# Kernel optimization log

Hardware: AMD Instinct MI355X
Metric: run time of the kernel (lower is better)

The kernel has to match this reference:

```python
import jax, jax.numpy as jnp
import numpy as np

B, T, I, H = 512, 512, 32, 64


def setup_inputs() -> dict:
    key = jax.random.key(0)
    ks = jax.random.split(key, 11)
    s_i = 1.0 / np.sqrt(H)  # PyTorch GRU init scale
    inp = {
        "x": jax.random.normal(ks[0], (B, T, I), dtype=jnp.float32),
        # layer 0 (input size I), layer 1 (input size H); gate order r,z,n
        "W_ih0": jax.random.uniform(ks[1], (3 * H, I), jnp.float32, -s_i, s_i),
        "W_hh0": jax.random.uniform(ks[2], (3 * H, H), jnp.float32, -s_i, s_i),
        "b_ih0": jax.random.uniform(ks[3], (3 * H,), jnp.float32, -s_i, s_i),
        "b_hh0": jax.random.uniform(ks[4], (3 * H,), jnp.float32, -s_i, s_i),
        "W_ih1": jax.random.uniform(ks[5], (3 * H, H), jnp.float32, -s_i, s_i),
        "W_hh1": jax.random.uniform(ks[6], (3 * H, H), jnp.float32, -s_i, s_i),
        "b_ih1": jax.random.uniform(ks[7], (3 * H,), jnp.float32, -s_i, s_i),
        "b_hh1": jax.random.uniform(ks[8], (3 * H,), jnp.float32, -s_i, s_i),
        "fc_w": jax.random.uniform(ks[9], (1, H), jnp.float32, -s_i, s_i),
        "fc_b": jax.random.uniform(ks[10], (1,), jnp.float32, -s_i, s_i),
    }
    return inp


def gru_layer(x, W_ih, W_hh, b_ih, b_hh):
    """One GRU layer over [B,T,D] -> [B,T,H]. PyTorch gate order r,z,n."""
    h = x.shape[-1] * 0  # placeholder, real H from W_hh
    H_ = W_hh.shape[1]
    # precompute input projections for all timesteps: [B,T,3H]
    gi = jnp.einsum("btd,gd->btg", x, W_ih) + b_ih
    gi = jnp.swapaxes(gi, 0, 1)  # [T,B,3H] for scan

    def step(h_prev, gi_t):
        gh = h_prev @ W_hh.T + b_hh  # [B,3H]
        i_r, i_z, i_n = jnp.split(gi_t, 3, axis=-1)
        h_r, h_z, h_n = jnp.split(gh, 3, axis=-1)
        r = jax.nn.sigmoid(i_r + h_r)
        z = jax.nn.sigmoid(i_z + h_z)
        n = jnp.tanh(i_n + r * h_n)
        h_new = (1.0 - z) * n + z * h_prev
        return h_new, h_new

    h0 = jnp.zeros((x.shape[0], H_), dtype=x.dtype)
    _, ys = jax.lax.scan(step, h0, gi)
    return jnp.swapaxes(ys, 0, 1)  # [B,T,H]


def reference(x, W_ih0, W_hh0, b_ih0, b_hh0, W_ih1, W_hh1, b_ih1, b_hh1, fc_w, fc_b):
    # dropout between layers is inactive in eval mode -> identity
    h1 = gru_layer(x, W_ih0, W_hh0, b_ih0, b_hh0)
    h2 = gru_layer(h1, W_ih1, W_hh1, b_ih1, b_hh1)
    last = h2[:, -1, :]  # [B,H]
    return last @ fc_w.T + fc_b  # [B,1]
```

## Files before the change

### kernel.cpp

```cpp
#include <hip/hip_runtime.h>

typedef _Float16 h2 __attribute__((ext_vector_type(2)));
typedef _Float16 h4 __attribute__((ext_vector_type(4)));
typedef _Float16 h8 __attribute__((ext_vector_type(8)));
typedef float    f4 __attribute__((ext_vector_type(4)));

#define TT 512
#define NB 512
#define II 32
#define HH 64
#define BT 16
#define LROW 72

static __device__ __forceinline__ float fexp2f(float x){ return __builtin_amdgcn_exp2f(x); }
static __device__ __forceinline__ float frcpf(float x){ return __builtin_amdgcn_rcpf(x); }
static __device__ __forceinline__ float sigf(float x){ return frcpf(1.0f + fexp2f(-1.442695040888963f*x)); }
static __device__ __forceinline__ float tanhf_fast(float x){ return 1.0f - 2.0f*frcpf(1.0f + fexp2f(2.885390081777926f*x)); }

struct H8S { h2 a,b,c,d; };
struct H4S { h2 a,b; };
static __device__ __forceinline__ h2 pkrtz(float a, float b){
  return __builtin_bit_cast(h2, __builtin_amdgcn_cvt_pkrtz(a, b));
}
static __device__ __forceinline__ h8 pack8(h2 a, h2 b, h2 c, h2 d){
  H8S s{a,b,c,d}; return __builtin_bit_cast(h8, s);
}
static __device__ __forceinline__ h8 cvt8(float4 a, float4 b){
  return pack8(pkrtz(a.x,a.y), pkrtz(a.z,a.w), pkrtz(b.x,b.y), pkrtz(b.z,b.w));
}
static __device__ __forceinline__ h8 ld8cvt(const float* p){
  return cvt8(((const float4*)p)[0], ((const float4*)p)[1]);
}
static __device__ __forceinline__ f4 mfma16(h8 a, h8 b, f4 c){
  return __builtin_amdgcn_mfma_f32_16x16x32_f16(a, b, c, 0, 0, 0);
}

static __device__ __forceinline__ void phase_barrier(){
  asm volatile("s_waitcnt lgkmcnt(0)" ::: "memory");
  __builtin_amdgcn_s_barrier();
  asm volatile("" ::: "memory");
}

#define GPHASE(DOL0, DOL1, XA, XB, P)                                        \
{                                                                            \
  const _Float16* h0r = &h0L[buf][c*LROW];                                   \
  h8 ba = *(const h8*)(h0r + 8*g);                                           \
  h8 bb = *(const h8*)(h0r + 32 + 8*g);                                      \
  f4 Dr, Dz, Dni, Dnh;                                                       \
  if (DOL1) {                                                                \
    const _Float16* h1r = &h1L[buf][c*LROW];                                 \
    h8 v0 = *(const h8*)(h1r + 8*g);                                         \
    h8 v1 = *(const h8*)(h1r + 32 + 8*g);                                    \
    Dr = brv1; Dz = bzv1; Dni = biv1; Dnh = bhv1;                            \
    Dr  = mfma16(P0[0][0], ba, Dr);   Dr  = mfma16(P0[0][1], bb, Dr);        \
    Dr  = mfma16(P1[0][0], v0, Dr);   Dr  = mfma16(P1[0][1], v1, Dr);        \
    Dz  = mfma16(P0[1][0], ba, Dz);   Dz  = mfma16(P0[1][1], bb, Dz);        \
    Dz  = mfma16(P1[1][0], v0, Dz);   Dz  = mfma16(P1[1][1], v1, Dz);        \
    Dni = mfma16(P0[2][0], ba, Dni);  Dni = mfma16(P0[2][1], bb, Dni);       \
    Dnh = mfma16(P1[2][0], v0, Dnh);  Dnh = mfma16(P1[2][1], v1, Dnh);       \
  }                                                                          \
  if (DOL0) {                                                                \
    h8 bx = cvt8(XA, XB);                                                    \
    f4 Cr = brv0, Cz = bzv0, Cni = biv0, Cnh = bhv0;                         \
    Cr  = mfma16(Ah[0][0], ba, Cr);   Cr  = mfma16(Ah[0][1], bb, Cr);        \
    Cz  = mfma16(Ah[1][0], ba, Cz);   Cz  = mfma16(Ah[1][1], bb, Cz);        \
    Cnh = mfma16(Ah[2][0], ba, Cnh);  Cnh = mfma16(Ah[2][1], bb, Cnh);       \
    Cr  = mfma16(Ax[0], bx, Cr);                                             \
    Cz  = mfma16(Ax[1], bx, Cz);                                             \
    Cni = mfma16(Ax[2], bx, Cni);                                            \
    { const float* pn = xrow + (size_t)(((P)+2 < TT) ? ((P)+2) : (TT-1))*II; \
      XA = ((const float4*)pn)[0];  XB = ((const float4*)pn)[1]; }           \
    _Pragma("unroll")                                                        \
    for (int i = 0; i < 4; ++i){                                             \
      const float r  = sigf(Cr[i]);                                          \
      const float z  = sigf(Cz[i]);                                          \
      const float nn = tanhf_fast(Cni[i] + r*Cnh[i]);                        \
      hp0[i] = nn + z*(hp0[i] - nn);                                         \
    }                                                                        \
    H4S s0{ pkrtz(hp0[0], hp0[1]), pkrtz(hp0[2], hp0[3]) };                  \
    *(h4*)(&h0L[buf^1][c*LROW + j0]) = __builtin_bit_cast(h4, s0);           \
  }                                                                          \
  if (DOL1) {                                                                \
    _Pragma("unroll")                                                        \
    for (int i = 0; i < 4; ++i){                                             \
      const float r  = sigf(Dr[i]);                                          \
      const float z  = sigf(Dz[i]);                                          \
      const float nn = tanhf_fast(Dni[i] + r*Dnh[i]);                        \
      hp1[i] = nn + z*(hp1[i] - nn);                                         \
    }                                                                        \
    H4S s1{ pkrtz(hp1[0], hp1[1]), pkrtz(hp1[2], hp1[3]) };                  \
    *(h4*)(&h1L[buf^1][c*LROW + j0]) = __builtin_bit_cast(h4, s1);           \
  }                                                                          \
  phase_barrier();                                                           \
  buf ^= 1;                                                                  \
}

__global__ __launch_bounds__(256, 1)
void gru2_merged(
    const float* __restrict__ x,
    const float* __restrict__ Wih0, const float* __restrict__ Whh0,
    const float* __restrict__ bih0, const float* __restrict__ bhh0,
    const float* __restrict__ Wih1, const float* __restrict__ Whh1,
    const float* __restrict__ b_ih1, const float* __restrict__ b_hh1,
    const float* __restrict__ fcw, const float* __restrict__ fcb,
    float* __restrict__ out)
{
  const int tid  = threadIdx.x;
  const int w    = tid >> 6;
  const int lane = tid & 63;
  const int c    = lane & 15;
  const int g    = lane >> 4;
  const int b0   = blockIdx.x * BT;

  __shared__ _Float16 h0L[2][16*LROW];
  __shared__ _Float16 h1L[2][16*LROW];
  __shared__ float    fcred[256];

  for (int i = tid; i < 16*LROW; i += 256){
    h0L[0][i] = (_Float16)0; h0L[1][i] = (_Float16)0;
    h1L[0][i] = (_Float16)0; h1L[1][i] = (_Float16)0;
  }

  const int r0 = 16*w + c, r1 = 64 + 16*w + c, r2 = 128 + 16*w + c;
  const int j0 = 16*w + 4*g;

  h8 Ax[3];
  h8 Ah[3][2];
  h8 P0[3][2];
  h8 P1[3][2];
  Ax[0] = ld8cvt(Wih0 + r0*II + 8*g);
  Ax[1] = ld8cvt(Wih0 + r1*II + 8*g);
  Ax[2] = ld8cvt(Wih0 + r2*II + 8*g);
#pragma unroll
  for (int q = 0; q < 2; ++q){
    Ah[0][q] = ld8cvt(Whh0 + r0*HH + 32*q + 8*g);
    Ah[1][q] = ld8cvt(Whh0 + r1*HH + 32*q + 8*g);
    Ah[2][q] = ld8cvt(Whh0 + r2*HH + 32*q + 8*g);
    P0[0][q] = ld8cvt(Wih1 + r0*HH + 32*q + 8*g);
    P0[1][q] = ld8cvt(Wih1 + r1*HH + 32*q + 8*g);
    P0[2][q] = ld8cvt(Wih1 + r2*HH + 32*q + 8*g);
    P1[0][q] = ld8cvt(Whh1 + r0*HH + 32*q + 8*g);
    P1[1][q] = ld8cvt(Whh1 + r1*HH + 32*q + 8*g);
    P1[2][q] = ld8cvt(Whh1 + r2*HH + 32*q + 8*g);
  }

  f4 brv0, bzv0, biv0, bhv0, brv1, bzv1, biv1, bhv1;
#pragma unroll
  for (int i = 0; i < 4; ++i){
    brv0[i] = bih0[j0+i]      + bhh0[j0+i];
    bzv0[i] = bih0[64+j0+i]   + bhh0[64+j0+i];
    biv0[i] = bih0[128+j0+i];
    bhv0[i] = bhh0[128+j0+i];
    brv1[i] = b_ih1[j0+i]     + b_hh1[j0+i];
    bzv1[i] = b_ih1[64+j0+i]  + b_hh1[64+j0+i];
    biv1[i] = b_ih1[128+j0+i];
    bhv1[i] = b_hh1[128+j0+i];
  }

  float hp0[4] = {0.f,0.f,0.f,0.f};
  float hp1[4] = {0.f,0.f,0.f,0.f};

  const float* xrow = x + (size_t)(b0+c)*TT*II + 8*g;
  float4 x0a, x0b, x1a, x1b;
  x0a = ((const float4*)xrow)[0];       x0b = ((const float4*)xrow)[1];
  x1a = ((const float4*)(xrow+II))[0];  x1b = ((const float4*)(xrow+II))[1];

  int buf = 0;
  __syncthreads();

  GPHASE(true, false, x0a, x0b, 0);
  for (int p = 1; p < TT-1; p += 2){
    GPHASE(true, true, x1a, x1b, p);
    GPHASE(true, true, x0a, x0b, p+1);
  }
  GPHASE(true, true, x1a, x1b, TT-1);
  GPHASE(false, true, x0a, x0b, 0);

  {
    float s = fcw[j0]*hp1[0] + fcw[j0+1]*hp1[1] + fcw[j0+2]*hp1[2] + fcw[j0+3]*hp1[3];
    fcred[(w*4 + g)*16 + c] = s;
  }
  __syncthreads();
  if (tid < 16){
    float s = fcb[0];
#pragma unroll
    for (int q = 0; q < 16; ++q) s += fcred[q*16 + tid];
    out[b0 + tid] = s;
  }
}

extern "C" void kernel_launch(void* const* d_in, const int* in_sizes, int n_in,
                              void* d_out, int out_size, void* d_ws, size_t ws_size,
                              hipStream_t stream) {
  const float* x    = (const float*)d_in[0];
  const float* Wih0 = (const float*)d_in[1];
  const float* Whh0 = (const float*)d_in[2];
  const float* bih0 = (const float*)d_in[3];
  const float* bhh0 = (const float*)d_in[4];
  const float* Wih1 = (const float*)d_in[5];
  const float* Whh1 = (const float*)d_in[6];
  const float* bih1 = (const float*)d_in[7];
  const float* bhh1 = (const float*)d_in[8];
  const float* fcw  = (const float*)d_in[9];
  const float* fcb  = (const float*)d_in[10];
  float* out = (float*)d_out;

  gru2_merged<<<dim3(NB/BT), dim3(256), 0, stream>>>(
      x, Wih0, Whh0, bih0, bhh0, Wih1, Whh1, bih1, bhh1, fcw, fcb, out);
}
```

Before: 313.1 us.

## Pack two batch groups per block and replace barriers with LDS flag sync

Each 512-thread block now runs two independent 4-wave groups, each handling 16 batch rows with its own LDS state buffers. The grid shrinks to half as many blocks, so two recurrence chains share one CU. The per-step s_barrier is replaced by a per-group spin on LDS flags, using monotonic phase counters and s_sleep, so one group never waits on the other. The aim is to hide each chain's serial latency by interleaving two chains on the same SIMDs. The cost is CU sharing and polling overhead, and the sleep may add wake-up latency to every step.

```diff
diff --git a/kernel.cpp b/kernel.cpp
--- a/kernel.cpp
+++ b/kernel.cpp
@@ -11,6 +11,7 @@
 #define HH 64
 #define BT 16
 #define LROW 72
+#define HSZ  (16*LROW)
 
 static __device__ __forceinline__ float fexp2f(float x){ return __builtin_amdgcn_exp2f(x); }
 static __device__ __forceinline__ float frcpf(float x){ return __builtin_amdgcn_rcpf(x); }
@@ -35,20 +36,23 @@
   return __builtin_amdgcn_mfma_f32_16x16x32_f16(a, b, c, 0, 0, 0);
 }
 
-static __device__ __forceinline__ void phase_barrier(){
+static __device__ __forceinline__ void group_sync(volatile int* fl, int wt, int lane, int target){
   asm volatile("s_waitcnt lgkmcnt(0)" ::: "memory");
-  __builtin_amdgcn_s_barrier();
+  if (lane == 0) fl[wt] = target;
+  while (!(fl[0] >= target && fl[1] >= target && fl[2] >= target && fl[3] >= target)) {
+    __builtin_amdgcn_s_sleep(1);
+  }
   asm volatile("" ::: "memory");
 }
 
 #define GPHASE(DOL0, DOL1, XA, XB, P)                                        \
 {                                                                            \
-  const _Float16* h0r = &h0L[buf][c*LROW];                                   \
+  const _Float16* h0r = h0B + (size_t)buf*HSZ + c*LROW;                      \
   h8 ba = *(const h8*)(h0r + 8*g);                                           \
   h8 bb = *(const h8*)(h0r + 32 + 8*g);                                      \
   f4 Dr, Dz, Dni, Dnh;                                                       \
   if (DOL1) {                                                                \
-    const _Float16* h1r = &h1L[buf][c*LROW];                                 \
+    const _Float16* h1r = h1B + (size_t)buf*HSZ + c*LROW;                    \
     h8 v0 = *(const h8*)(h1r + 8*g);                                         \
     h8 v1 = *(const h8*)(h1r + 32 + 8*g);                                    \
     Dr = brv1; Dz = bzv1; Dni = biv1; Dnh = bhv1;                            \
@@ -78,7 +82,7 @@
       hp0[i] = nn + z*(hp0[i] - nn);                                         \
     }                                                                        \
     H4S s0{ pkrtz(hp0[0], hp0[1]), pkrtz(hp0[2], hp0[3]) };                  \
-    *(h4*)(&h0L[buf^1][c*LROW + j0]) = __builtin_bit_cast(h4, s0);           \
+    *(h4*)(h0B + (size_t)(buf^1)*HSZ + c*LROW + j0) = __builtin_bit_cast(h4, s0); \
   }                                                                          \
   if (DOL1) {                                                                \
     _Pragma("unroll")                                                        \
@@ -89,14 +93,15 @@
       hp1[i] = nn + z*(hp1[i] - nn);                                         \
     }                                                                        \
     H4S s1{ pkrtz(hp1[0], hp1[1]), pkrtz(hp1[2], hp1[3]) };                  \
-    *(h4*)(&h1L[buf^1][c*LROW + j0]) = __builtin_bit_cast(h4, s1);           \
+    *(h4*)(h1B + (size_t)(buf^1)*HSZ + c*LROW + j0) = __builtin_bit_cast(h4, s1); \
   }                                                                          \
-  phase_barrier();                                                           \
+  ++ph;                                                                      \
+  group_sync(flg, wt, lane, ph);                                             \
   buf ^= 1;                                                                  \
 }
 
-__global__ __launch_bounds__(256, 1)
-void gru2_merged(
+__global__ __launch_bounds__(512, 2)
+void gru2_dual(
     const float* __restrict__ x,
     const float* __restrict__ Wih0, const float* __restrict__ Whh0,
     const float* __restrict__ bih0, const float* __restrict__ bhh0,
@@ -107,22 +112,31 @@
 {
   const int tid  = threadIdx.x;
   const int w    = tid >> 6;
+  const int grp  = w >> 2;
+  const int wt   = w & 3;
   const int lane = tid & 63;
   const int c    = lane & 15;
   const int g    = lane >> 4;
-  const int b0   = blockIdx.x * BT;
-
-  __shared__ _Float16 h0L[2][16*LROW];
-  __shared__ _Float16 h1L[2][16*LROW];
-  __shared__ float    fcred[256];
-
-  for (int i = tid; i < 16*LROW; i += 256){
-    h0L[0][i] = (_Float16)0; h0L[1][i] = (_Float16)0;
-    h1L[0][i] = (_Float16)0; h1L[1][i] = (_Float16)0;
-  }
-
-  const int r0 = 16*w + c, r1 = 64 + 16*w + c, r2 = 128 + 16*w + c;
-  const int j0 = 16*w + 4*g;
+  const int b0   = blockIdx.x * (2*BT) + grp*BT;
+
+  __shared__ _Float16 h0G[2][2][HSZ];
+  __shared__ _Float16 h1G[2][2][HSZ];
+  __shared__ float    fcred[2][256];
+  __shared__ int      flags[2][4];
+
+  for (int i = tid; i < 2*2*HSZ; i += 512){
+    ((_Float16*)h0G)[i] = (_Float16)0;
+    ((_Float16*)h1G)[i] = (_Float16)0;
+  }
+  if (tid < 8) ((int*)flags)[tid] = 0;
+
+  _Float16* h0B = &h0G[grp][0][0];
+  _Float16* h1B = &h1G[grp][0][0];
+  volatile int* flg = &flags[grp][0];
+  int ph = 0;
+
+  const int r0 = 16*wt + c, r1 = 64 + 16*wt + c, r2 = 128 + 16*wt + c;
+  const int j0 = 16*wt + 4*g;
 
   h8 Ax[3];
   h8 Ah[3][2];
@@ -178,14 +192,15 @@
 
   {
     float s = fcw[j0]*hp1[0] + fcw[j0+1]*hp1[1] + fcw[j0+2]*hp1[2] + fcw[j0+3]*hp1[3];
-    fcred[(w*4 + g)*16 + c] = s;
-  }
-  __syncthreads();
-  if (tid < 16){
+    fcred[grp][(wt*4 + g)*16 + c] = s;
+  }
+  ++ph;
+  group_sync(flg, wt, lane, ph);
+  if (wt == 0 && lane < 16){
     float s = fcb[0];
 #pragma unroll
-    for (int q = 0; q < 16; ++q) s += fcred[q*16 + tid];
-    out[b0 + tid] = s;
+    for (int q = 0; q < 16; ++q) s += fcred[grp][q*16 + lane];
+    out[b0 + lane] = s;
   }
 }
 
@@ -205,6 +220,6 @@
   const float* fcb  = (const float*)d_in[10];
   float* out = (float*)d_out;
 
-  gru2_merged<<<dim3(NB/BT), dim3(256), 0, stream>>>(
+  gru2_dual<<<dim3(NB/(2*BT)), dim3(512), 0, stream>>>(
       x, Wih0, Whh0, bih0, bhh0, Wih1, Whh1, bih1, bhh1, fcw, fcb, out);
 }
```

After: 570.3 us. 82.1% more time.
